# Kernel optimization log

Measured on AMD Instinct MI355X. Metric: run time of the kernel, lower is better.

Reference implementation:

```python
import jax, jax.numpy as jnp
import numpy as np

B, C, S, H, W = 1, 256, 64, 32, 128
BLOCKS, HEADS, DH = 2, 8, 32
SCALE = DH ** (-0.5)


def layer_norm(x, w, b, eps=1e-5):
    mu = jnp.mean(x, axis=-1, keepdims=True)
    var = jnp.var(x, axis=-1, keepdims=True)
    return (x - mu) * jax.lax.rsqrt(var + eps) * w + b


def generate_y_for_attn(y, u):
    # y: (B,C,H,W), u: (B,S,S) float -> (B, S^2, 2H, C)
    Bv, Cv, Hv, Wv = y.shape
    Sv = u.shape[1]
    uf = jnp.floor(u).reshape(Bv, Sv * Sv)
    u_left = jnp.clip(uf, 0, Wv - 1).astype(jnp.int32)
    u_right = jnp.clip(uf + 1, 0, Wv - 1).astype(jnp.int32)
    yf = y.reshape(Bv, Cv * Hv, Wv)

    def gather_w(idx):
        idxb = jnp.broadcast_to(idx[:, None, :], (Bv, Cv * Hv, Sv * Sv))
        return jnp.take_along_axis(yf, idxb, axis=2).reshape(Bv, Cv, Hv, Sv * Sv)

    ys = jnp.concatenate([gather_w(u_left), gather_w(u_right)], axis=2)  # (B,C,2H,S2)
    return ys.transpose(0, 3, 2, 1)  # (B, S2, 2H, C)


def cross_attention(x, y, p, i):
    # x: (B,M,C), y: (B,M,N,C)
    q = layer_norm(x, p['ln_q_w'][i], p['ln_q_b'][i]) @ p['Wq'][i]        # (B,M,HD)
    k = layer_norm(y, p['ln_k_w'][i], p['ln_k_b'][i]) @ p['Wk'][i]        # (B,M,N,HD)
    v = layer_norm(y, p['ln_v_w'][i], p['ln_v_b'][i]) @ p['Wv'][i]        # (B,M,N,HD)
    Bv, M, _ = q.shape
    N = k.shape[2]
    q = q.reshape(Bv, M, HEADS, DH)
    k = k.reshape(Bv, M, N, HEADS, DH)
    v = v.reshape(Bv, M, N, HEADS, DH)
    dot = SCALE * jnp.einsum('bmhd,bmnhd->bhmn', q, k)                    # (B,H,M,N)
    attn = jax.nn.softmax(dot, axis=-1)
    a = jnp.einsum('bhmn,bmnhd->bmhd', attn, v).reshape(Bv, M, HEADS * DH)
    z = a @ p['Wproj'][i] + p['bproj'][i]
    z = layer_norm(z, p['ln_pre_w'][i], p['ln_pre_b'][i])
    h = jax.nn.gelu(z @ p['Wm1'][i] + p['bm1'][i], approximate=False)
    z = z + (h @ p['Wm2'][i] + p['bm2'][i])
    return layer_norm(z, p['ln_post_w'][i], p['ln_post_b'][i])


def setup_inputs() -> dict:
    key = jax.random.key(0)
    ks = jax.random.split(key, 16)
    std = 0.02
    inp = {
        'grd2sat': jax.random.normal(ks[0], (B, C, S, S), jnp.float32),
        'grd_x': jax.random.normal(ks[1], (B, C, H, W), jnp.float32),
        'u': jax.random.uniform(ks[2], (B, S, S), jnp.float32) * (W - 1),
        'ln_q_w': jnp.ones((BLOCKS, C)), 'ln_q_b': jnp.zeros((BLOCKS, C)),
        'ln_k_w': jnp.ones((BLOCKS, C)), 'ln_k_b': jnp.zeros((BLOCKS, C)),
        'ln_v_w': jnp.ones((BLOCKS, C)), 'ln_v_b': jnp.zeros((BLOCKS, C)),
        'Wq': std * jax.random.normal(ks[3], (BLOCKS, C, HEADS * DH)),
        'Wk': std * jax.random.normal(ks[4], (BLOCKS, C, HEADS * DH)),
        'Wv': std * jax.random.normal(ks[5], (BLOCKS, C, HEADS * DH)),
        'Wproj': std * jax.random.normal(ks[6], (BLOCKS, HEADS * DH, C)),
        'bproj': jnp.zeros((BLOCKS, C)),
        'ln_pre_w': jnp.ones((BLOCKS, C)), 'ln_pre_b': jnp.zeros((BLOCKS, C)),
        'Wm1': std * jax.random.normal(ks[7], (BLOCKS, C, 2 * C)),
        'bm1': jnp.zeros((BLOCKS, 2 * C)),
        'Wm2': std * jax.random.normal(ks[8], (BLOCKS, 2 * C, C)),
        'bm2': jnp.zeros((BLOCKS, C)),
        'ln_post_w': jnp.ones((BLOCKS, C)), 'ln_post_b': jnp.zeros((BLOCKS, C)),
    }
    return inp


def reference(grd2sat, grd_x, u, ln_q_w, ln_q_b, ln_k_w, ln_k_b, ln_v_w, ln_v_b,
              Wq, Wk, Wv, Wproj, bproj, ln_pre_w, ln_pre_b, Wm1, bm1, Wm2, bm2,
              ln_post_w, ln_post_b):
    p = dict(ln_q_w=ln_q_w, ln_q_b=ln_q_b, ln_k_w=ln_k_w, ln_k_b=ln_k_b,
             ln_v_w=ln_v_w, ln_v_b=ln_v_b, Wq=Wq, Wk=Wk, Wv=Wv, Wproj=Wproj,
             bproj=bproj, ln_pre_w=ln_pre_w, ln_pre_b=ln_pre_b, Wm1=Wm1, bm1=bm1,
             Wm2=Wm2, bm2=bm2, ln_post_w=ln_post_w, ln_post_b=ln_post_b)
    y_attn = generate_y_for_attn(grd_x, u)               # (B, S^2, 2H, C)
    x = grd2sat.reshape(B, C, S * S).transpose(0, 2, 1)  # (B, M, C)
    for i in range(BLOCKS):
        # (Swin self-attention layer omitted; cross-attention stack only.)
        x = cross_attention(x, y_attn, p, i)
    out = x.transpose(0, 2, 1).reshape(B, C, S, S)
    # L2 normalize over channel dim
    norm = jnp.sqrt(jnp.sum(out * out, axis=1, keepdims=True))
    return out / jnp.maximum(norm, 1e-12)
```

## Files before the change

kernel.cpp:

```cpp
#include <hip/hip_runtime.h>
#include <math.h>


#define C_DIM 256
#define M_DIM 4096
#define W_DIM 128
#define H_DIM 32
#define ATT_SCALE 0.17677669529663687f

typedef __attribute__((ext_vector_type(8))) short short8;
typedef __attribute__((ext_vector_type(4))) short short4v;
typedef __attribute__((ext_vector_type(4))) float floatx4;

__device__ __forceinline__ unsigned short f2bf(float f) {
    unsigned u = __float_as_uint(f);
    unsigned r = (u + 0x7fffu + ((u >> 16) & 1u)) >> 16;
    return (unsigned short)r;
}
__device__ __forceinline__ float gelu_exact(float x) {
    return 0.5f * x * (1.0f + erff(x * 0.70710678118654752f));
}

struct PrepArgs {
    const float* grd2sat; float* xcur;
    const float* grd_x;   float* yhat;
    const float* u; int* perm; int4* chunks; int* nchunks;
    const float* win[12]; unsigned short* wout[12]; const float* wlnw[12];
    int wR[12], wC[12], wbase[13];
    const float* fW[10]; const float* flnb[10]; const float* fbase[10];
    float* fout[10];
    int fN[10], fwcol[10], focol[10];
};

__global__ __launch_bounds__(256) void prep_kernel(PrepArgs a) {
    __shared__ float smemf[9024];
    int b = blockIdx.x, t = threadIdx.x;
    if (b < 256) {
        float (*tile)[65] = (float(*)[65])smemf;
        int m0 = (b & 63) << 6, c0 = (b >> 6) << 6;
        for (int it = 0; it < 16; ++it) {
            int idx = it * 256 + t;
            int co = idx >> 6, mo = idx & 63;
            tile[co][mo] = a.grd2sat[(size_t)(c0 + co) * M_DIM + m0 + mo];
        }
        __syncthreads();
        for (int it = 0; it < 16; ++it) {
            int idx = it * 256 + t;
            int mo = idx >> 6, co = idx & 63;
            a.xcur[(size_t)(m0 + mo) * C_DIM + c0 + co] = tile[co][mo];
        }
    } else if (b < 384) {
        int idx = b - 256;
        int h = idx & 31, w0 = (idx >> 5) << 5;
        float (*tile)[33] = (float(*)[33])smemf;
        float (*ps)[32] = (float(*)[32])(smemf + 8448);
        float (*pss)[32] = (float(*)[32])(smemf + 8704);
        float* mu_s = smemf + 8960;
        float* rs_s = smemf + 8992;
        int wo = t & 31, cb = t >> 5;
        for (int it = 0; it < 32; ++it) {
            int c = it * 8 + cb;
            tile[c][wo] = a.grd_x[(size_t)c * (H_DIM * W_DIM) + h * W_DIM + w0 + wo];
        }
        __syncthreads();
        {
            int w = t & 31, part = t >> 5;
            float s = 0.f, ss = 0.f;
            for (int c = part * 32; c < part * 32 + 32; ++c) {
                float x = tile[c][w];
                s += x; ss += x * x;
            }
            ps[part][w] = s; pss[part][w] = ss;
        }
        __syncthreads();
        if (t < 32) {
            float s = 0.f, ss = 0.f;
            for (int p = 0; p < 8; ++p) { s += ps[p][t]; ss += pss[p][t]; }
            float mu = s * (1.f / 256.f);
            float var = ss * (1.f / 256.f) - mu * mu;
            mu_s[t] = mu;
            rs_s[t] = rsqrtf(var + 1e-5f);
        }
        __syncthreads();
        for (int jj = 0; jj < 32; ++jj) {
            float mu = mu_s[jj], rs = rs_s[jj];
            a.yhat[((size_t)(w0 + jj) * H_DIM + h) * C_DIM + t] =
                (tile[t][jj] - mu) * rs;
        }
    } else if (b < 1408) {
        int wI = b - 384;
        int e = 0;
        while (wI >= a.wbase[e + 1]) ++e;
        int tl = wI - a.wbase[e];
        int tilesC = a.wC[e] >> 5;
        int tr = tl / tilesC, tc = tl - tr * tilesC;
        int r0 = tr << 5, c0 = tc << 5;
        const float* in = a.win[e];
        unsigned short* out = a.wout[e];
        const float* lnw = a.wlnw[e];
        int R = a.wR[e], Cc = a.wC[e];
        float (*tile)[33] = (float(*)[33])smemf;
        int rl = t >> 3, cq = (t & 7) << 2;
        float4 v = *(const float4*)&in[(size_t)(r0 + rl) * Cc + c0 + cq];
        if (lnw) {
            float s = lnw[r0 + rl];
            v.x *= s; v.y *= s; v.z *= s; v.w *= s;
        }
        tile[rl][cq + 0] = v.x;
        tile[rl][cq + 1] = v.y;
        tile[rl][cq + 2] = v.z;
        tile[rl][cq + 3] = v.w;
        __syncthreads();
        int cl = t >> 3, rq = (t & 7) << 2;
        ushort4 o;
        o.x = f2bf(tile[rq + 0][cl]);
        o.y = f2bf(tile[rq + 1][cl]);
        o.z = f2bf(tile[rq + 2][cl]);
        o.w = f2bf(tile[rq + 3][cl]);
        *(ushort4*)&out[(size_t)(c0 + cl) * R + r0 + rq] = o;
    } else if (b < 1448) {
        int idx = b - 1408;
        int jj = idx >> 2, part = idx & 3;
        int N = a.fN[jj];
        int c = t & 63, kp = t >> 6;
        int wcol = a.fwcol[jj] + (part << 6) + c;
        const float* W = a.fW[jj];
        const float* lb = a.flnb[jj];
        float s = 0.f;
        for (int k = kp * 64; k < kp * 64 + 64; ++k)
            s += lb[k] * W[(size_t)k * N + wcol];
        smemf[(kp << 6) + c] = s;
        __syncthreads();
        if (t < 64) {
            float tot = smemf[t] + smemf[64 + t] + smemf[128 + t] + smemf[192 + t];
            int ocol = a.focol[jj] + (part << 6) + t;
            if (a.fbase[jj]) tot += a.fbase[jj][a.fwcol[jj] + (part << 6) + t];
            a.fout[jj][ocol] = tot;
        }
    } else {
        int* hist = (int*)smemf;
        int* cur = (int*)smemf + 128;
        unsigned short* wlb = (unsigned short*)((int*)smemf + 256);
        if (t < 128) hist[t] = 0;
        __syncthreads();
        for (int it = 0; it < 16; ++it) {
            int m = it * 256 + t;
            int wl = (int)floorf(a.u[m]);
            wl = max(0, min(wl, 126));
            wlb[m] = (unsigned short)wl;
            atomicAdd(&hist[wl], 1);
        }
        __syncthreads();
        if (t == 0) {
            int run = 0, nc = 0;
            for (int bkt = 0; bkt < 127; ++bkt) {
                int c = hist[bkt];
                cur[bkt] = run;
                int q0 = run;
                while (c > 0) {
                    int take = min(c, 32);
                    a.chunks[nc] = make_int4(bkt, q0, take, 0);
                    ++nc; q0 += take; c -= take;
                }
                run += hist[bkt];
            }
            *a.nchunks = nc;
        }
        __syncthreads();
        for (int it = 0; it < 16; ++it) {
            int m = it * 256 + t;
            int wl = wlb[m];
            int pos = atomicAdd(&cur[wl], 1);
            a.perm[pos] = m;
        }
    }
}

struct GJ {
    const void* A; const unsigned short* Bt;
    const float* bias;
    void* out; unsigned short* out2;
    int K, N;
};

__device__ __forceinline__ void gemm_core_kv(const GJ& j, short (*As)[264],
                                             short (*Bs)[264], int bm, int by) {
    int t = threadIdx.x;
    int bn = by << 6;
    int wv = t >> 6, lane = t & 63;
    int mt = wv & 1, nt0 = (wv >> 1) << 1;
    int quad = lane >> 4, l16 = lane & 15;
    floatx4 acc0 = {0.f, 0.f, 0.f, 0.f};
    floatx4 acc1 = {0.f, 0.f, 0.f, 0.f};
    {
        int ar = t >> 3, cq = (t & 7) << 2;
        const float* ap = (const float*)j.A + (size_t)(bm + ar) * 256 + cq;
        float4 v[8];
#pragma unroll
        for (int g = 0; g < 8; ++g) v[g] = *(const float4*)(ap + g * 32);
#pragma unroll
        for (int g = 0; g < 8; ++g) {
            short4v o;
            o[0] = (short)f2bf(v[g].x);
            o[1] = (short)f2bf(v[g].y);
            o[2] = (short)f2bf(v[g].z);
            o[3] = (short)f2bf(v[g].w);
            *(short4v*)&As[ar][cq + g * 32] = o;
        }
    }
    {
        int br = t >> 2, cq2 = (t & 3) << 3;
        const unsigned short* bp = j.Bt + (size_t)(bn + br) * 256 + cq2;
#pragma unroll
        for (int g = 0; g < 8; ++g)
            *(short8*)&Bs[br][cq2 + g * 32] = *(const short8*)(bp + g * 32);
    }
    __syncthreads();
#pragma unroll
    for (int k0 = 0; k0 < 8; ++k0) {
        short8 aa = *(const short8*)&As[(mt << 4) + l16][(k0 << 5) + (quad << 3)];
        short8 b0 = *(const short8*)&Bs[(nt0 << 4) + l16][(k0 << 5) + (quad << 3)];
        short8 b1 =
            *(const short8*)&Bs[((nt0 + 1) << 4) + l16][(k0 << 5) + (quad << 3)];
        acc0 = __builtin_amdgcn_mfma_f32_16x16x32_bf16(aa, b0, acc0, 0, 0, 0);
        acc1 = __builtin_amdgcn_mfma_f32_16x16x32_bf16(aa, b1, acc1, 0, 0, 0);
    }
#pragma unroll
    for (int jj = 0; jj < 2; ++jj) {
        const floatx4 accv = jj ? acc1 : acc0;
        int col = bn + ((nt0 + jj) << 4) + l16;
        float bv = j.bias[col];
#pragma unroll
        for (int r = 0; r < 4; ++r) {
            int row = bm + (mt << 4) + (quad << 2) + r;
            float v = accv[r] + bv;
            if (col < 256)
                ((unsigned short*)j.out)[(size_t)row * 256 + col] = f2bf(v);
            else
                j.out2[(size_t)(col - 256) * M_DIM + row] = f2bf(v);
        }
    }
}

__global__ __launch_bounds__(256) void kv_kernel(GJ j0, GJ j1) {
    __shared__ short As[32][264];
    __shared__ short Bs[64][264];
    int bm = blockIdx.x << 5;
    if ((int)blockIdx.y < 8)
        gemm_core_kv(j0, As, Bs, bm, blockIdx.y);
    else
        gemm_core_kv(j1, As, Bs, bm, blockIdx.y - 8);
}

struct MegaArgs {
    const float* xcur;
    const int* perm; const int4* chunks; const int* nchunks;
    float* xfinal;
    const unsigned short* Wq[2]; const unsigned short* Wp[2];
    const unsigned short* Wm1[2]; const unsigned short* Wm2[2];
    const unsigned short* Ktb[2]; const unsigned short* Vtb[2];
    const float* qb[2]; const float* m1b[2];
    const float* bpj[2]; const float* bm2v[2];
    const float* pw[2]; const float* pb[2];
    const float* aw; const float* ab;
};

struct BPre { short8 b[8][2]; };

__device__ __forceinline__ void preloadB(const unsigned short* Bt, int Kstride,
                                         int koff, int colw, int l16, int quad,
                                         BPre& P) {
    const unsigned short* bp =
        Bt + (size_t)(colw + l16) * Kstride + koff + (quad << 3);
#pragma unroll
    for (int k0 = 0; k0 < 8; ++k0)
#pragma unroll
        for (int ni = 0; ni < 2; ++ni)
            P.b[k0][ni] =
                *(const short8*)(bp + (size_t)(ni << 4) * Kstride + (k0 << 5));
}

__device__ __forceinline__ void mfma32t(const short* As, int lda, const BPre& P,
                                        int l16, int quad, floatx4 acc[2][2]) {
    const short* ap = As + (size_t)l16 * lda + (quad << 3);
#pragma unroll
    for (int k0 = 0; k0 < 8; ++k0) {
        short8 a0 = *(const short8*)(ap + (k0 << 5));
        short8 a1 = *(const short8*)(ap + (size_t)16 * lda + (k0 << 5));
        acc[0][0] = __builtin_amdgcn_mfma_f32_16x16x32_bf16(a0, P.b[k0][0], acc[0][0], 0, 0, 0);
        acc[0][1] = __builtin_amdgcn_mfma_f32_16x16x32_bf16(a0, P.b[k0][1], acc[0][1], 0, 0, 0);
        acc[1][0] = __builtin_amdgcn_mfma_f32_16x16x32_bf16(a1, P.b[k0][0], acc[1][0], 0, 0, 0);
        acc[1][1] = __builtin_amdgcn_mfma_f32_16x16x32_bf16(a1, P.b[k0][1], acc[1][1], 0, 0, 0);
    }
}

#define ZACC(A) \
    { A[0][0] = (floatx4){0.f,0.f,0.f,0.f}; A[0][1] = (floatx4){0.f,0.f,0.f,0.f}; \
      A[1][0] = (floatx4){0.f,0.f,0.f,0.f}; A[1][1] = (floatx4){0.f,0.f,0.f,0.f}; }

__global__ __launch_bounds__(512) void mega_kernel(MegaArgs a) {
    __shared__ __align__(16) char smem[137856];
    short (*XH)[264] = (short(*)[264])(smem);
    short (*QR)[264] = (short(*)[264])(smem + 16896);
    short (*ZH)[264] = (short(*)[264])(smem + 33792);
    short (*AR)[264] = (short(*)[264])(smem + 50688);
    float (*Zf)[260] = (float(*)[260])(smem + 67584);
    short (*PB)[32][72] = (short(*)[32][72])(smem + 100864);
    int* gp = (int*)(smem + 137728);

    if ((int)blockIdx.x >= *a.nchunks) return;
    int4 cd = a.chunks[blockIdx.x];
    int wl = cd.x, qstart = cd.y, qcnt = cd.z;
    int t = threadIdx.x;
    if (t < 32) gp[t] = (t < qcnt) ? a.perm[qstart + t] : a.perm[qstart];
    __syncthreads();

    int wv = t >> 6, lane = t & 63, quad = lane >> 4, l16 = lane & 15;
    int colw = wv << 5;
    int r16 = t >> 4, c0 = (t & 15) << 4;

#pragma unroll 1
    for (int l = 0; l < 2; ++l) {
        BPre Pq;
        preloadB(a.Wq[l], 256, 0, colw, l16, quad, Pq);
        {
            float4 v[4];
            if (l == 0) {
                const float* xp = a.xcur + (size_t)gp[r16] * 256 + c0;
#pragma unroll
                for (int g4 = 0; g4 < 4; ++g4)
                    v[g4] = *(const float4*)(xp + (g4 << 2));
            } else {
#pragma unroll
                for (int g4 = 0; g4 < 4; ++g4)
                    v[g4] = *(const float4*)&Zf[r16][c0 + (g4 << 2)];
            }
            float s = 0.f, ss = 0.f;
#pragma unroll
            for (int g4 = 0; g4 < 4; ++g4) {
                s += v[g4].x + v[g4].y + v[g4].z + v[g4].w;
                ss += v[g4].x * v[g4].x + v[g4].y * v[g4].y + v[g4].z * v[g4].z +
                      v[g4].w * v[g4].w;
            }
#pragma unroll
            for (int o = 1; o < 16; o <<= 1) {
                s += __shfl_xor(s, o, 64);
                ss += __shfl_xor(ss, o, 64);
            }
            float mu = s * (1.f / 256.f);
            float rs = rsqrtf(ss * (1.f / 256.f) - mu * mu + 1e-5f);
#pragma unroll
            for (int g4 = 0; g4 < 4; ++g4) {
                v[g4].x = (v[g4].x - mu) * rs;
                v[g4].y = (v[g4].y - mu) * rs;
                v[g4].z = (v[g4].z - mu) * rs;
                v[g4].w = (v[g4].w - mu) * rs;
            }
            if (l == 1) {
                float s2 = 0.f, ss2 = 0.f;
#pragma unroll
                for (int g4 = 0; g4 < 4; ++g4) {
                    float4 w4 = *(const float4*)&a.aw[c0 + (g4 << 2)];
                    float4 b4 = *(const float4*)&a.ab[c0 + (g4 << 2)];
                    v[g4].x = v[g4].x * w4.x + b4.x;
                    v[g4].y = v[g4].y * w4.y + b4.y;
                    v[g4].z = v[g4].z * w4.z + b4.z;
                    v[g4].w = v[g4].w * w4.w + b4.w;
                    s2 += v[g4].x + v[g4].y + v[g4].z + v[g4].w;
                    ss2 += v[g4].x * v[g4].x + v[g4].y * v[g4].y +
                           v[g4].z * v[g4].z + v[g4].w * v[g4].w;
                }
#pragma unroll
                for (int o = 1; o < 16; o <<= 1) {
                    s2 += __shfl_xor(s2, o, 64);
                    ss2 += __shfl_xor(ss2, o, 64);
                }
                float mu2 = s2 * (1.f / 256.f);
                float rs2 = rsqrtf(ss2 * (1.f / 256.f) - mu2 * mu2 + 1e-5f);
#pragma unroll
                for (int g4 = 0; g4 < 4; ++g4) {
                    v[g4].x = (v[g4].x - mu2) * rs2;
                    v[g4].y = (v[g4].y - mu2) * rs2;
                    v[g4].z = (v[g4].z - mu2) * rs2;
                    v[g4].w = (v[g4].w - mu2) * rs2;
                }
            }
#pragma unroll
            for (int g4 = 0; g4 < 4; ++g4) {
                short4v o;
                o[0] = (short)f2bf(v[g4].x);
                o[1] = (short)f2bf(v[g4].y);
                o[2] = (short)f2bf(v[g4].z);
                o[3] = (short)f2bf(v[g4].w);
                *(short4v*)&XH[r16][c0 + (g4 << 2)] = o;
            }
        }
        __syncthreads();

        short8 kb[4], vfrag[2][2];
        {
            const unsigned short* Kt = a.Ktb[l];
            const unsigned short* Vt = a.Vtb[l];
            int h = wv;
#pragma unroll
            for (int nt = 0; nt < 4; ++nt)
                kb[nt] = *(const short8*)(
                    Kt + (size_t)((wl << 5) + (nt << 4) + l16) * 256 +
                    (h << 5) + (quad << 3));
#pragma unroll
            for (int ks = 0; ks < 2; ++ks)
#pragma unroll
                for (int dt = 0; dt < 2; ++dt)
                    vfrag[ks][dt] = *(const short8*)(
                        Vt + (size_t)((h << 5) + (dt << 4) + l16) * M_DIM +
                        (wl << 5) + (ks << 5) + (quad << 3));
        }
        {
            floatx4 acc[2][2];
            ZACC(acc);
            mfma32t((const short*)XH, 264, Pq, l16, quad, acc);
            const float* qb = a.qb[l];
#pragma unroll
            for (int ni = 0; ni < 2; ++ni) {
                int col = colw + (ni << 4) + l16;
                float bv = qb[col];
#pragma unroll
                for (int mi = 0; mi < 2; ++mi)
#pragma unroll
                    for (int r = 0; r < 4; ++r)
                        QR[(mi << 4) + (quad << 2) + r][col] =
                            (short)f2bf(acc[mi][ni][r] + bv);
            }
        }
        __syncthreads();

        BPre Pp;
        {
            int h = wv;
            short8 aq0 = *(const short8*)&QR[l16][(h << 5) + (quad << 3)];
            short8 aq1 = *(const short8*)&QR[16 + l16][(h << 5) + (quad << 3)];
            floatx4 c[2][4];
#pragma unroll
            for (int nt = 0; nt < 4; ++nt) {
                floatx4 z = {0.f, 0.f, 0.f, 0.f};
                c[0][nt] = __builtin_amdgcn_mfma_f32_16x16x32_bf16(aq0, kb[nt], z, 0, 0, 0);
                c[1][nt] = __builtin_amdgcn_mfma_f32_16x16x32_bf16(aq1, kb[nt], z, 0, 0, 0);
            }
            floatx4 ri[2];
#pragma unroll
            for (int m = 0; m < 2; ++m) {
#pragma unroll
                for (int nt = 0; nt < 4; ++nt) {
                    floatx4 e;
#pragma unroll
                    for (int r = 0; r < 4; ++r)
                        e[r] = __expf(c[m][nt][r] * ATT_SCALE);
                    c[m][nt] = e;
                }
                floatx4 s4 = c[m][0] + c[m][1] + c[m][2] + c[m][3];
#pragma unroll
                for (int r = 0; r < 4; ++r) {
                    float s = s4[r];
                    s += __shfl_xor(s, 1, 64);
                    s += __shfl_xor(s, 2, 64);
                    s += __shfl_xor(s, 4, 64);
                    s += __shfl_xor(s, 8, 64);
                    ri[m][r] = 1.f / s;
                }
            }
#pragma unroll
            for (int m = 0; m < 2; ++m)
#pragma unroll
                for (int nt = 0; nt < 4; ++nt)
#pragma unroll
                    for (int r = 0; r < 4; ++r)
                        PB[wv][(m << 4) + (quad << 2) + r][(nt << 4) + l16] =
                            (short)f2bf(c[m][nt][r] * ri[m][r]);
            __threadfence_block();
            preloadB(a.Wp[l], 256, 0, colw, l16, quad, Pp);
            floatx4 o[2][2];
#pragma unroll
            for (int m = 0; m < 2; ++m)
#pragma unroll
                for (int dt = 0; dt < 2; ++dt)
                    o[m][dt] = (floatx4){0.f, 0.f, 0.f, 0.f};
#pragma unroll
            for (int ks = 0; ks < 2; ++ks) {
                short8 pa0 =
                    *(const short8*)&PB[wv][l16][(ks << 5) + (quad << 3)];
                short8 pa1 =
                    *(const short8*)&PB[wv][16 + l16][(ks << 5) + (quad << 3)];
#pragma unroll
                for (int dt = 0; dt < 2; ++dt) {
                    o[0][dt] = __builtin_amdgcn_mfma_f32_16x16x32_bf16(
                        pa0, vfrag[ks][dt], o[0][dt], 0, 0, 0);
                    o[1][dt] = __builtin_amdgcn_mfma_f32_16x16x32_bf16(
                        pa1, vfrag[ks][dt], o[1][dt], 0, 0, 0);
                }
            }
            int h5 = wv << 5;
#pragma unroll
            for (int m = 0; m < 2; ++m)
#pragma unroll
                for (int dt = 0; dt < 2; ++dt)
#pragma unroll
                    for (int r = 0; r < 4; ++r)
                        AR[(m << 4) + (quad << 2) + r]
                          [h5 + (dt << 4) + l16] = (short)f2bf(o[m][dt][r]);
        }
        __syncthreads();

        {
            floatx4 acc[2][2];
            ZACC(acc);
            mfma32t((const short*)AR, 264, Pp, l16, quad, acc);
            const float* bpj = a.bpj[l];
#pragma unroll
            for (int ni = 0; ni < 2; ++ni) {
                int col = colw + (ni << 4) + l16;
                float bv = bpj[col];
#pragma unroll
                for (int mi = 0; mi < 2; ++mi)
#pragma unroll
                    for (int r = 0; r < 4; ++r)
                        Zf[(mi << 4) + (quad << 2) + r][col] = acc[mi][ni][r] + bv;
            }
        }
        __syncthreads();

        BPre Pm1a;
        preloadB(a.Wm1[l], 256, 0, colw, l16, quad, Pm1a);
        {
            const float* pw = a.pw[l];
            const float* pb = a.pb[l];
            float4 v[4];
#pragma unroll
            for (int g4 = 0; g4 < 4; ++g4)
                v[g4] = *(const float4*)&Zf[r16][c0 + (g4 << 2)];
            float s = 0.f, ss = 0.f;
#pragma unroll
            for (int g4 = 0; g4 < 4; ++g4) {
                s += v[g4].x + v[g4].y + v[g4].z + v[g4].w;
                ss += v[g4].x * v[g4].x + v[g4].y * v[g4].y + v[g4].z * v[g4].z +
                      v[g4].w * v[g4].w;
            }
#pragma unroll
            for (int o = 1; o < 16; o <<= 1) {
                s += __shfl_xor(s, o, 64);
                ss += __shfl_xor(ss, o, 64);
            }
            float mu = s * (1.f / 256.f);
            float rs = rsqrtf(ss * (1.f / 256.f) - mu * mu + 1e-5f);
#pragma unroll
            for (int g4 = 0; g4 < 4; ++g4) {
                float4 z;
                z.x = (v[g4].x - mu) * rs;
                z.y = (v[g4].y - mu) * rs;
                z.z = (v[g4].z - mu) * rs;
                z.w = (v[g4].w - mu) * rs;
                short4v o;
                o[0] = (short)f2bf(z.x);
                o[1] = (short)f2bf(z.y);
                o[2] = (short)f2bf(z.z);
                o[3] = (short)f2bf(z.w);
                *(short4v*)&ZH[r16][c0 + (g4 << 2)] = o;
                float4 w4 = *(const float4*)&pw[c0 + (g4 << 2)];
                float4 b4 = *(const float4*)&pb[c0 + (g4 << 2)];
                float4 za;
                za.x = z.x * w4.x + b4.x;
                za.y = z.y * w4.y + b4.y;
                za.z = z.z * w4.z + b4.z;
                za.w = z.w * w4.w + b4.w;
                *(float4*)&Zf[r16][c0 + (g4 << 2)] = za;
            }
        }
        __syncthreads();

        const float* m1b = a.m1b[l];
        BPre Pm2a;
        {
            floatx4 acc[2][2];
            ZACC(acc);
            mfma32t((const short*)ZH, 264, Pm1a, l16, quad, acc);
            BPre Pm1b;
            preloadB(a.Wm1[l] + (size_t)256 * 256, 256, 0, colw, l16, quad, Pm1b);
#pragma unroll
            for (int ni = 0; ni < 2; ++ni) {
                int col = colw + (ni << 4) + l16;
                float bv = m1b[col];
#pragma unroll
                for (int mi = 0; mi < 2; ++mi)
#pragma unroll
                    for (int r = 0; r < 4; ++r)
                        XH[(mi << 4) + (quad << 2) + r][col] =
                            (short)f2bf(gelu_exact(acc[mi][ni][r] + bv));
            }
            floatx4 acc2[2][2];
            ZACC(acc2);
            mfma32t((const short*)ZH, 264, Pm1b, l16, quad, acc2);
            preloadB(a.Wm2[l], 512, 0, colw, l16, quad, Pm2a);
#pragma unroll
            for (int ni = 0; ni < 2; ++ni) {
                int col = colw + (ni << 4) + l16;
                float bv = m1b[256 + col];
#pragma unroll
                for (int mi = 0; mi < 2; ++mi)
#pragma unroll
                    for (int r = 0; r < 4; ++r)
                        QR[(mi << 4) + (quad << 2) + r][col] =
                            (short)f2bf(gelu_exact(acc2[mi][ni][r] + bv));
            }
        }
        __syncthreads();

        {
            floatx4 macc[2][2];
            ZACC(macc);
            mfma32t((const short*)XH, 264, Pm2a, l16, quad, macc);
            BPre Pm2b;
            preloadB(a.Wm2[l], 512, 256, colw, l16, quad, Pm2b);
            mfma32t((const short*)QR, 264, Pm2b, l16, quad, macc);
            const float* b2 = a.bm2v[l];
#pragma unroll
            for (int ni = 0; ni < 2; ++ni) {
                int col = colw + (ni << 4) + l16;
                float bv = b2[col];
#pragma unroll
                for (int mi = 0; mi < 2; ++mi)
#pragma unroll
                    for (int r = 0; r < 4; ++r) {
                        int row = (mi << 4) + (quad << 2) + r;
                        float v = macc[mi][ni][r] + bv + Zf[row][col];
                        if (l == 0) {
                            Zf[row][col] = v;
                        } else if (row < qcnt) {
                            a.xfinal[(size_t)gp[row] * 256 + col] = v;
                        }
                    }
            }
        }
        __syncthreads();
    }
}

__global__ __launch_bounds__(256) void out_kernel(const float* __restrict__ X,
                                                  const float* __restrict__ w,
                                                  const float* __restrict__ b,
                                                  float* __restrict__ out) {
    __shared__ float tile[64][65];
    int t = threadIdx.x;
    int mo = t >> 2, q = t & 3;
    int m0 = blockIdx.x << 6;
    const float* p = X + (size_t)(m0 + mo) * C_DIM + (q << 6);
    float4 v[16];
    float s = 0.f, ss = 0.f;
#pragma unroll
    for (int c = 0; c < 16; ++c) {
        v[c] = *(const float4*)(p + c * 4);
        s += v[c].x + v[c].y + v[c].z + v[c].w;
        ss += v[c].x * v[c].x + v[c].y * v[c].y + v[c].z * v[c].z + v[c].w * v[c].w;
    }
    s += __shfl_xor(s, 1, 64); s += __shfl_xor(s, 2, 64);
    ss += __shfl_xor(ss, 1, 64); ss += __shfl_xor(ss, 2, 64);
    float mu = s * (1.f / 256.f);
    float rs = rsqrtf(ss * (1.f / 256.f) - mu * mu + 1e-5f);
    float ss2 = 0.f;
#pragma unroll
    for (int c = 0; c < 16; ++c) {
        float4 w4 = *(const float4*)&w[(q << 6) + c * 4];
        float4 b4 = *(const float4*)&b[(q << 6) + c * 4];
        v[c].x = (v[c].x - mu) * rs * w4.x + b4.x;
        v[c].y = (v[c].y - mu) * rs * w4.y + b4.y;
        v[c].z = (v[c].z - mu) * rs * w4.z + b4.z;
        v[c].w = (v[c].w - mu) * rs * w4.w + b4.w;
        ss2 += v[c].x * v[c].x + v[c].y * v[c].y + v[c].z * v[c].z + v[c].w * v[c].w;
    }
    ss2 += __shfl_xor(ss2, 1, 64); ss2 += __shfl_xor(ss2, 2, 64);
    float sc = 1.f / fmaxf(sqrtf(ss2), 1e-12f);
    for (int cc = 0; cc < 4; ++cc) {
        if (q == cc) {
#pragma unroll
            for (int c = 0; c < 16; ++c) {
                tile[mo][c * 4 + 0] = v[c].x * sc;
                tile[mo][c * 4 + 1] = v[c].y * sc;
                tile[mo][c * 4 + 2] = v[c].z * sc;
                tile[mo][c * 4 + 3] = v[c].w * sc;
            }
        }
        __syncthreads();
        for (int it = 0; it < 16; ++it) {
            int idx = it * 256 + t;
            int co = idx >> 6, mr = idx & 63;
            out[(size_t)((cc << 6) + co) * M_DIM + m0 + mr] = tile[mr][co];
        }
        __syncthreads();
    }
}

extern "C" void kernel_launch(void* const* d_in, const int* in_sizes, int n_in,
                              void* d_out, int out_size, void* d_ws, size_t ws_size,
                              hipStream_t stream) {
    const float* grd2sat = (const float*)d_in[0];
    const float* grd_x   = (const float*)d_in[1];
    const float* u       = (const float*)d_in[2];
    const float* ln_q_w  = (const float*)d_in[3];
    const float* ln_q_b  = (const float*)d_in[4];
    const float* ln_k_w  = (const float*)d_in[5];
    const float* ln_k_b  = (const float*)d_in[6];
    const float* ln_v_w  = (const float*)d_in[7];
    const float* ln_v_b  = (const float*)d_in[8];
    const float* Wq      = (const float*)d_in[9];
    const float* Wk      = (const float*)d_in[10];
    const float* Wv      = (const float*)d_in[11];
    const float* Wproj   = (const float*)d_in[12];
    const float* bproj   = (const float*)d_in[13];
    const float* ln_pre_w = (const float*)d_in[14];
    const float* ln_pre_b = (const float*)d_in[15];
    const float* Wm1     = (const float*)d_in[16];
    const float* bm1     = (const float*)d_in[17];
    const float* Wm2     = (const float*)d_in[18];
    const float* bm2     = (const float*)d_in[19];
    const float* ln_post_w = (const float*)d_in[20];
    const float* ln_post_b = (const float*)d_in[21];

    float* ws   = (float*)d_ws;
    float* yhat = ws;
    float* xcur = ws + 1048576;
    float* zq   = ws + 2097152;
    unsigned short* Ktab0 = (unsigned short*)(ws + 6291456);
    unsigned short* Vt0   = (unsigned short*)(ws + 6815744);
    unsigned short* Ktab1 = (unsigned short*)(ws + 7340032);
    unsigned short* Vt1   = (unsigned short*)(ws + 7864320);
    unsigned short* Bt    = (unsigned short*)(ws + 8388608);
    float* biasbuf = ws + 8912896;
    int*  perm    = (int*)(ws + 8915456);
    int4* chunks  = (int4*)(ws + 8919552);
    int*  nchunks = (int*)(ws + 8921600);
    const size_t BS = 524288;
    const size_t OQ = 0, OKV = 65536, OP = 196608, OM1 = 262144, OM2 = 393216;

    dim3 b256(256);

    PrepArgs pa;
    pa.grd2sat = grd2sat; pa.xcur = xcur;
    pa.grd_x = grd_x;     pa.yhat = yhat;
    pa.u = u; pa.perm = perm; pa.chunks = chunks; pa.nchunks = nchunks;
    {
        int base = 0;
        for (int i = 0; i < 2; ++i) {
            int e = 6 * i;
            unsigned short* bt = Bt + i * BS;
            pa.win[e+0] = Wq + i * 65536;    pa.wout[e+0] = bt + OQ;
            pa.wlnw[e+0] = ln_q_w + i * 256; pa.wR[e+0] = 256; pa.wC[e+0] = 256;
            pa.win[e+1] = Wk + i * 65536;    pa.wout[e+1] = bt + OKV;
            pa.wlnw[e+1] = ln_k_w + i * 256; pa.wR[e+1] = 256; pa.wC[e+1] = 256;
            pa.win[e+2] = Wv + i * 65536;    pa.wout[e+2] = bt + OKV + 65536;
            pa.wlnw[e+2] = ln_v_w + i * 256; pa.wR[e+2] = 256; pa.wC[e+2] = 256;
            pa.win[e+3] = Wproj + i * 65536; pa.wout[e+3] = bt + OP;
            pa.wlnw[e+3] = nullptr;          pa.wR[e+3] = 256; pa.wC[e+3] = 256;
            pa.win[e+4] = Wm1 + i * 131072;  pa.wout[e+4] = bt + OM1;
            pa.wlnw[e+4] = ln_pre_w + i * 256; pa.wR[e+4] = 256; pa.wC[e+4] = 512;
            pa.win[e+5] = Wm2 + i * 131072;  pa.wout[e+5] = bt + OM2;
            pa.wlnw[e+5] = nullptr;          pa.wR[e+5] = 512; pa.wC[e+5] = 256;
        }
        for (int e = 0; e < 12; ++e) {
            pa.wbase[e] = base;
            base += (pa.wR[e] >> 5) * (pa.wC[e] >> 5);
        }
        pa.wbase[12] = base;
        for (int i = 0; i < 2; ++i) {
            int jb = 5 * i;
            float* bb = biasbuf + i * 1280;
            pa.fW[jb+0] = Wq + i * 65536; pa.flnb[jb+0] = ln_q_b + i * 256;
            pa.fbase[jb+0] = nullptr; pa.fout[jb+0] = bb;
            pa.fN[jb+0] = 256; pa.fwcol[jb+0] = 0; pa.focol[jb+0] = 0;
            pa.fW[jb+1] = Wk + i * 65536; pa.flnb[jb+1] = ln_k_b + i * 256;
            pa.fbase[jb+1] = nullptr; pa.fout[jb+1] = bb + 256;
            pa.fN[jb+1] = 256; pa.fwcol[jb+1] = 0; pa.focol[jb+1] = 0;
            pa.fW[jb+2] = Wv + i * 65536; pa.flnb[jb+2] = ln_v_b + i * 256;
            pa.fbase[jb+2] = nullptr; pa.fout[jb+2] = bb + 256;
            pa.fN[jb+2] = 256; pa.fwcol[jb+2] = 0; pa.focol[jb+2] = 256;
            pa.fW[jb+3] = Wm1 + i * 131072; pa.flnb[jb+3] = ln_pre_b + i * 256;
            pa.fbase[jb+3] = bm1 + i * 512; pa.fout[jb+3] = bb + 768;
            pa.fN[jb+3] = 512; pa.fwcol[jb+3] = 0; pa.focol[jb+3] = 0;
            pa.fW[jb+4] = Wm1 + i * 131072; pa.flnb[jb+4] = ln_pre_b + i * 256;
            pa.fbase[jb+4] = bm1 + i * 512; pa.fout[jb+4] = bb + 768;
            pa.fN[jb+4] = 512; pa.fwcol[jb+4] = 256; pa.focol[jb+4] = 256;
        }
    }
    prep_kernel<<<1449, b256, 0, stream>>>(pa);

    GJ jkv0 = {};
    jkv0.A = yhat; jkv0.Bt = Bt + OKV; jkv0.bias = biasbuf + 256;
    jkv0.out = Ktab0; jkv0.out2 = Vt0; jkv0.K = 256; jkv0.N = 512;
    GJ jkv1 = {};
    jkv1.A = yhat; jkv1.Bt = Bt + BS + OKV; jkv1.bias = biasbuf + 1280 + 256;
    jkv1.out = Ktab1; jkv1.out2 = Vt1; jkv1.K = 256; jkv1.N = 512;
    kv_kernel<<<dim3(128, 16), b256, 0, stream>>>(jkv0, jkv1);

    MegaArgs ma;
    ma.xcur = xcur; ma.perm = perm; ma.chunks = chunks; ma.nchunks = nchunks;
    ma.xfinal = zq;
    for (int i = 0; i < 2; ++i) {
        const unsigned short* bt = Bt + i * BS;
        ma.Wq[i] = bt + OQ; ma.Wp[i] = bt + OP;
        ma.Wm1[i] = bt + OM1; ma.Wm2[i] = bt + OM2;
        ma.Ktb[i] = i ? Ktab1 : Ktab0; ma.Vtb[i] = i ? Vt1 : Vt0;
        ma.qb[i] = biasbuf + i * 1280;
        ma.m1b[i] = biasbuf + i * 1280 + 768;
        ma.bpj[i] = bproj + i * 256;
        ma.bm2v[i] = bm2 + i * 256;
        ma.pw[i] = ln_pre_w + i * 256;
        ma.pb[i] = ln_pre_b + i * 256;
    }
    ma.aw = ln_post_w; ma.ab = ln_post_b;
    mega_kernel<<<288, dim3(512), 0, stream>>>(ma);

    out_kernel<<<64, b256, 0, stream>>>(zq, ln_post_w + 256, ln_post_b + 256,
                                        (float*)d_out);
}
```

Baseline: 207.1 us.

## Store normalized y in bf16, hoist weight preloads, retile output kernel

The normalized y buffer now holds bf16 instead of fp32, so the KV GEMM loads bf16 A tiles directly with no per-tile conversion, and the buffer's write and read traffic is halved. In the mega kernel, weight B-fragment preloads move earlier so they overlap the preceding compute, and the next layer's Wq is prefetched. The output kernel processes 32 rows per block over 128 blocks, with one shared-memory tile pass replacing four synchronized passes. The earlier preloads keep more registers live, which may cut occupancy.

```diff
diff --git a/kernel.cpp b/kernel.cpp
--- a/kernel.cpp
+++ b/kernel.cpp
@@ -4,8 +4,6 @@
 
 #define C_DIM 256
 #define M_DIM 4096
-#define W_DIM 128
-#define H_DIM 32
 #define ATT_SCALE 0.17677669529663687f
 
 typedef __attribute__((ext_vector_type(8))) short short8;
@@ -23,7 +21,7 @@
 
 struct PrepArgs {
     const float* grd2sat; float* xcur;
-    const float* grd_x;   float* yhat;
+    const float* grd_x;   unsigned short* yhat;
     const float* u; int* perm; int4* chunks; int* nchunks;
     const float* win[12]; unsigned short* wout[12]; const float* wlnw[12];
     int wR[12], wC[12], wbase[13];
@@ -60,7 +58,7 @@
         int wo = t & 31, cb = t >> 5;
         for (int it = 0; it < 32; ++it) {
             int c = it * 8 + cb;
-            tile[c][wo] = a.grd_x[(size_t)c * (H_DIM * W_DIM) + h * W_DIM + w0 + wo];
+            tile[c][wo] = a.grd_x[(size_t)c * 4096 + h * 128 + w0 + wo];
         }
         __syncthreads();
         {
@@ -84,8 +82,8 @@
         __syncthreads();
         for (int jj = 0; jj < 32; ++jj) {
             float mu = mu_s[jj], rs = rs_s[jj];
-            a.yhat[((size_t)(w0 + jj) * H_DIM + h) * C_DIM + t] =
-                (tile[t][jj] - mu) * rs;
+            a.yhat[((size_t)(w0 + jj) * 32 + h) * C_DIM + t] =
+                f2bf((tile[t][jj] - mu) * rs);
         }
     } else if (b < 1408) {
         int wI = b - 384;
@@ -127,6 +125,7 @@
         const float* W = a.fW[jj];
         const float* lb = a.flnb[jj];
         float s = 0.f;
+#pragma unroll 4
         for (int k = kp * 64; k < kp * 64 + 64; ++k)
             s += lb[k] * W[(size_t)k * N + wcol];
         smemf[(kp << 6) + c] = s;
@@ -193,20 +192,12 @@
     floatx4 acc0 = {0.f, 0.f, 0.f, 0.f};
     floatx4 acc1 = {0.f, 0.f, 0.f, 0.f};
     {
-        int ar = t >> 3, cq = (t & 7) << 2;
-        const float* ap = (const float*)j.A + (size_t)(bm + ar) * 256 + cq;
-        float4 v[8];
-#pragma unroll
-        for (int g = 0; g < 8; ++g) v[g] = *(const float4*)(ap + g * 32);
-#pragma unroll
-        for (int g = 0; g < 8; ++g) {
-            short4v o;
-            o[0] = (short)f2bf(v[g].x);
-            o[1] = (short)f2bf(v[g].y);
-            o[2] = (short)f2bf(v[g].z);
-            o[3] = (short)f2bf(v[g].w);
-            *(short4v*)&As[ar][cq + g * 32] = o;
-        }
+        int ar = t >> 3, cq = (t & 7) << 5;
+        const unsigned short* ap =
+            (const unsigned short*)j.A + (size_t)(bm + ar) * 256 + cq;
+#pragma unroll
+        for (int c = 0; c < 4; ++c)
+            *(uint4*)&As[ar][cq + (c << 3)] = *(const uint4*)(ap + (c << 3));
     }
     {
         int br = t >> 2, cq2 = (t & 3) << 3;
@@ -319,10 +310,11 @@
     int colw = wv << 5;
     int r16 = t >> 4, c0 = (t & 15) << 4;
 
+    BPre Pq;
+    preloadB(a.Wq[0], 256, 0, colw, l16, quad, Pq);
+
 #pragma unroll 1
     for (int l = 0; l < 2; ++l) {
-        BPre Pq;
-        preloadB(a.Wq[l], 256, 0, colw, l16, quad, Pq);
         {
             float4 v[4];
             if (l == 0) {
@@ -435,6 +427,7 @@
         __syncthreads();
 
         BPre Pp;
+        preloadB(a.Wp[l], 256, 0, colw, l16, quad, Pp);
         {
             int h = wv;
             short8 aq0 = *(const short8*)&QR[l16][(h << 5) + (quad << 3)];
@@ -477,7 +470,6 @@
                         PB[wv][(m << 4) + (quad << 2) + r][(nt << 4) + l16] =
                             (short)f2bf(c[m][nt][r] * ri[m][r]);
             __threadfence_block();
-            preloadB(a.Wp[l], 256, 0, colw, l16, quad, Pp);
             floatx4 o[2][2];
 #pragma unroll
             for (int m = 0; m < 2; ++m)
@@ -510,6 +502,8 @@
         }
         __syncthreads();
 
+        BPre Pm1a;
+        preloadB(a.Wm1[l], 256, 0, colw, l16, quad, Pm1a);
         {
             floatx4 acc[2][2];
             ZACC(acc);
@@ -528,8 +522,6 @@
         }
         __syncthreads();
 
-        BPre Pm1a;
-        preloadB(a.Wm1[l], 256, 0, colw, l16, quad, Pm1a);
         {
             const float* pw = a.pw[l];
             const float* pb = a.pb[l];
@@ -579,11 +571,12 @@
         const float* m1b = a.m1b[l];
         BPre Pm2a;
         {
+            BPre Pm1b;
+            preloadB(a.Wm1[l] + (size_t)256 * 256, 256, 0, colw, l16, quad,
+                     Pm1b);
             floatx4 acc[2][2];
             ZACC(acc);
             mfma32t((const short*)ZH, 264, Pm1a, l16, quad, acc);
-            BPre Pm1b;
-            preloadB(a.Wm1[l] + (size_t)256 * 256, 256, 0, colw, l16, quad, Pm1b);
 #pragma unroll
             for (int ni = 0; ni < 2; ++ni) {
                 int col = colw + (ni << 4) + l16;
@@ -595,10 +588,10 @@
                         XH[(mi << 4) + (quad << 2) + r][col] =
                             (short)f2bf(gelu_exact(acc[mi][ni][r] + bv));
             }
+            preloadB(a.Wm2[l], 512, 0, colw, l16, quad, Pm2a);
             floatx4 acc2[2][2];
             ZACC(acc2);
             mfma32t((const short*)ZH, 264, Pm1b, l16, quad, acc2);
-            preloadB(a.Wm2[l], 512, 0, colw, l16, quad, Pm2a);
 #pragma unroll
             for (int ni = 0; ni < 2; ++ni) {
                 int col = colw + (ni << 4) + l16;
@@ -614,11 +607,11 @@
         __syncthreads();
 
         {
+            BPre Pm2b;
+            preloadB(a.Wm2[l], 512, 256, colw, l16, quad, Pm2b);
             floatx4 macc[2][2];
             ZACC(macc);
             mfma32t((const short*)XH, 264, Pm2a, l16, quad, macc);
-            BPre Pm2b;
-            preloadB(a.Wm2[l], 512, 256, colw, l16, quad, Pm2b);
             mfma32t((const short*)QR, 264, Pm2b, l16, quad, macc);
             const float* b2 = a.bm2v[l];
 #pragma unroll
@@ -638,6 +631,8 @@
                         }
                     }
             }
+            if (l == 0)
+                preloadB(a.Wq[1], 256, 0, colw, l16, quad, Pq);
         }
         __syncthreads();
     }
@@ -647,53 +642,49 @@
                                                   const float* __restrict__ w,
                                                   const float* __restrict__ b,
                                                   float* __restrict__ out) {
-    __shared__ float tile[64][65];
+    __shared__ float tile[32][261];
     int t = threadIdx.x;
-    int mo = t >> 2, q = t & 3;
-    int m0 = blockIdx.x << 6;
-    const float* p = X + (size_t)(m0 + mo) * C_DIM + (q << 6);
-    float4 v[16];
+    int mo = t >> 3, q = t & 7;
+    int m0 = blockIdx.x << 5;
+    const float* p = X + (size_t)(m0 + mo) * C_DIM + (q << 5);
+    float4 v[8];
     float s = 0.f, ss = 0.f;
 #pragma unroll
-    for (int c = 0; c < 16; ++c) {
+    for (int c = 0; c < 8; ++c) {
         v[c] = *(const float4*)(p + c * 4);
         s += v[c].x + v[c].y + v[c].z + v[c].w;
         ss += v[c].x * v[c].x + v[c].y * v[c].y + v[c].z * v[c].z + v[c].w * v[c].w;
     }
-    s += __shfl_xor(s, 1, 64); s += __shfl_xor(s, 2, 64);
-    ss += __shfl_xor(ss, 1, 64); ss += __shfl_xor(ss, 2, 64);
+    s += __shfl_xor(s, 1, 64); s += __shfl_xor(s, 2, 64); s += __shfl_xor(s, 4, 64);
+    ss += __shfl_xor(ss, 1, 64); ss += __shfl_xor(ss, 2, 64); ss += __shfl_xor(ss, 4, 64);
     float mu = s * (1.f / 256.f);
     float rs = rsqrtf(ss * (1.f / 256.f) - mu * mu + 1e-5f);
     float ss2 = 0.f;
 #pragma unroll
-    for (int c = 0; c < 16; ++c) {
-        float4 w4 = *(const float4*)&w[(q << 6) + c * 4];
-        float4 b4 = *(const float4*)&b[(q << 6) + c * 4];
+    for (int c = 0; c < 8; ++c) {
+        float4 w4 = *(const float4*)&w[(q << 5) + c * 4];
+        float4 b4 = *(const float4*)&b[(q << 5) + c * 4];
         v[c].x = (v[c].x - mu) * rs * w4.x + b4.x;
         v[c].y = (v[c].y - mu) * rs * w4.y + b4.y;
         v[c].z = (v[c].z - mu) * rs * w4.z + b4.z;
         v[c].w = (v[c].w - mu) * rs * w4.w + b4.w;
         ss2 += v[c].x * v[c].x + v[c].y * v[c].y + v[c].z * v[c].z + v[c].w * v[c].w;
     }
-    ss2 += __shfl_xor(ss2, 1, 64); ss2 += __shfl_xor(ss2, 2, 64);
+    ss2 += __shfl_xor(ss2, 1, 64); ss2 += __shfl_xor(ss2, 2, 64); ss2 += __shfl_xor(ss2, 4, 64);
     float sc = 1.f / fmaxf(sqrtf(ss2), 1e-12f);
-    for (int cc = 0; cc < 4; ++cc) {
-        if (q == cc) {
-#pragma unroll
-            for (int c = 0; c < 16; ++c) {
-                tile[mo][c * 4 + 0] = v[c].x * sc;
-                tile[mo][c * 4 + 1] = v[c].y * sc;
-                tile[mo][c * 4 + 2] = v[c].z * sc;
-                tile[mo][c * 4 + 3] = v[c].w * sc;
-            }
-        }
-        __syncthreads();
-        for (int it = 0; it < 16; ++it) {
-            int idx = it * 256 + t;
-            int co = idx >> 6, mr = idx & 63;
-            out[(size_t)((cc << 6) + co) * M_DIM + m0 + mr] = tile[mr][co];
-        }
-        __syncthreads();
+#pragma unroll
+    for (int c = 0; c < 8; ++c) {
+        tile[mo][(q << 5) + c * 4 + 0] = v[c].x * sc;
+        tile[mo][(q << 5) + c * 4 + 1] = v[c].y * sc;
+        tile[mo][(q << 5) + c * 4 + 2] = v[c].z * sc;
+        tile[mo][(q << 5) + c * 4 + 3] = v[c].w * sc;
+    }
+    __syncthreads();
+#pragma unroll 1
+    for (int it = 0; it < 32; ++it) {
+        int idx = it * 256 + t;
+        int c = idx >> 5, m = idx & 31;
+        out[(size_t)c * M_DIM + m0 + m] = tile[m][c];
     }
 }
 
@@ -724,7 +715,7 @@
     const float* ln_post_b = (const float*)d_in[21];
 
     float* ws   = (float*)d_ws;
-    float* yhat = ws;
+    unsigned short* yhat = (unsigned short*)ws;
     float* xcur = ws + 1048576;
     float* zq   = ws + 2097152;
     unsigned short* Ktab0 = (unsigned short*)(ws + 6291456);
@@ -816,6 +807,6 @@
     ma.aw = ln_post_w; ma.ab = ln_post_b;
     mega_kernel<<<288, dim3(512), 0, stream>>>(ma);
 
-    out_kernel<<<64, b256, 0, stream>>>(zq, ln_post_w + 256, ln_post_b + 256,
-                                        (float*)d_out);
-}
+    out_kernel<<<128, b256, 0, stream>>>(zq, ln_post_w + 256, ln_post_b + 256,
+                                         (float*)d_out);
+}
```

Result: slower. 211.8 us (+2.3%).
